# Performance work log

Hardware: AMD Instinct MI355X
Metric: run time of the kernel (lower is better)

Reference implementation:

```python
import jax, jax.numpy as jnp
import numpy as np

NHEAD = 16
D_MODEL = 1024
HEAD_DIM = D_MODEL // NHEAD


def setup_inputs() -> dict:
    key = jax.random.key(0)
    k1, k2, k3 = jax.random.split(key, 3)
    x = jax.random.normal(k1, (4, 2048, D_MODEL), dtype=jnp.float32)
    # lecun_normal-like scaling for stability
    w_qkv = jax.random.normal(k2, (D_MODEL, 3 * D_MODEL), dtype=jnp.float32) / np.sqrt(D_MODEL)
    w_out = jax.random.normal(k3, (D_MODEL, D_MODEL), dtype=jnp.float32) / np.sqrt(D_MODEL)
    return {"x": x, "w_qkv": w_qkv, "w_out": w_out}


def reference(x, w_qkv, w_out):
    # Fused QKV projection (self-attention: x_kv = x)
    qkv = x @ w_qkv  # [B, S, 3*D]
    q, k, v = jnp.split(qkv, 3, axis=-1)
    B, S = x.shape[0], x.shape[1]
    # [B, S, H, hd] -> [B, H, S, hd]
    q = jnp.moveaxis(q.reshape(B, S, NHEAD, HEAD_DIM), -2, -3)
    k = jnp.moveaxis(k.reshape(B, S, NHEAD, HEAD_DIM), -2, -3)
    v = jnp.moveaxis(v.reshape(B, S, NHEAD, HEAD_DIM), -2, -3)
    scale = 1.0 / jnp.sqrt(jnp.float32(HEAD_DIM))
    logits = jnp.einsum('bhqd,bhkd->bhqk', q, k) * scale
    weights = jax.nn.softmax(logits, axis=-1)
    out = jnp.einsum('bhqk,bhkd->bhqd', weights, v)  # [B, H, S, hd]
    out = jnp.moveaxis(out, -3, -2).reshape(B, S, D_MODEL)
    return out @ w_out
```

## Files before the change

kernel.cpp:

```cpp
#include <hip/hip_runtime.h>
#include <hip/hip_bf16.h>
#include <math.h>

#define D_MODEL 1024
#define NHEAD   16
#define HEAD_DIM 64
#define BATCH   4
#define SEQ     2048

typedef __attribute__((ext_vector_type(8))) short bf16x8;
typedef __attribute__((ext_vector_type(4))) float f32x4;
typedef __attribute__((ext_vector_type(16))) float f32x16;

__device__ inline ushort f2bf(float f) {
  __hip_bfloat16 h = __float2bfloat16(f);
  return *reinterpret_cast<ushort*>(&h);
}
__device__ inline uint pk2(float a, float b) {
  return (uint)f2bf(a) | ((uint)f2bf(b) << 16);
}
__device__ inline float bf2f(ushort u) {
  return __uint_as_float((uint)u << 16);
}
__device__ inline f32x16 zero16() {
  f32x16 z;
#pragma unroll
  for (int i = 0; i < 16; ++i) z[i] = 0.f;
  return z;
}
__device__ inline float fexp2(float x) { return __builtin_amdgcn_exp2f(x); }

__device__ inline void gld_lds16(const ushort* g, ushort* l) {
  __builtin_amdgcn_global_load_lds(
      (const __attribute__((address_space(1))) void*)g,
      (__attribute__((address_space(3))) void*)l, 16, 0, 0);
}

__global__ __launch_bounds__(256) void fill_f32(float* __restrict__ p, int n, float v) {
  int i = blockIdx.x * 256 + threadIdx.x;
  if (i < n) p[i] = v;
}

__global__ __launch_bounds__(256) void cast_bf16(const float* __restrict__ in,
                                                 ushort* __restrict__ out, int n8) {
  int i = blockIdx.x * 256 + threadIdx.x;
  if (i >= n8) return;
  const float4* p = (const float4*)(in + i * 8);
  float4 a = p[0], b = p[1];
  uint4 o;
  o.x = pk2(a.x, a.y); o.y = pk2(a.z, a.w);
  o.z = pk2(b.x, b.y); o.w = pk2(b.z, b.w);
  ((uint4*)out)[i] = o;
}

__global__ __launch_bounds__(256) void transpose_f32_bf16(const float* __restrict__ in,
                                                          ushort* __restrict__ out,
                                                          int R, int C) {
  __shared__ float tile[32][33];
  int tx = threadIdx.x, ty = threadIdx.y;
  int c0 = blockIdx.x * 32, r0 = blockIdx.y * 32;
#pragma unroll
  for (int k = 0; k < 4; ++k)
    tile[ty + 8 * k][tx] = in[(size_t)(r0 + ty + 8 * k) * C + c0 + tx];
  __syncthreads();
#pragma unroll
  for (int k = 0; k < 4; ++k)
    out[(size_t)(c0 + ty + 8 * k) * R + r0 + tx] = f2bf(tile[tx][ty + 8 * k]);
}

__device__ inline bf16x8 lds_read_swz(const ushort* base, int byteoff) {
  byteoff ^= ((byteoff >> 7) & 7) << 4;
  return *(const bf16x8*)((const char*)base + byteoff);
}

template <typename OutT>
__global__ __launch_bounds__(512, 2) void gemm_8ph(const ushort* __restrict__ A,
                                                   const ushort* __restrict__ BT,
                                                   OutT* __restrict__ C,
                                                   int M, int N, int K, int n_tiles) {
  __shared__ ushort AS[2][256 * 64];
  __shared__ ushort BS[2][256 * 64];

  const int tid = threadIdx.x;
  const int w = tid >> 6, lane = tid & 63;
  const int quad = lane >> 4, l16 = lane & 15;
  const int wm = w >> 2, wn = w & 3;
  const int tiles_x = N >> 8;
  const int NKT = K >> 6;

  int arow[4], acol[4];
  uint sdst[4];
#pragma unroll
  for (int i = 0; i < 4; ++i) {
    int x = (i * 512 + tid) * 16;
    int sx = x ^ (((x >> 7) & 7) << 4);
    arow[i] = sx >> 7;
    acol[i] = (sx & 127) >> 1;
    sdst[i] = (uint)(i * 512 + w * 64) * 8;
  }

  for (int t = blockIdx.x; t < n_tiles; t += gridDim.x) {
    const int m0 = (t / tiles_x) << 8, n0 = (t % tiles_x) << 8;

    int aoff[4], boff[4];
#pragma unroll
    for (int i = 0; i < 4; ++i) {
      aoff[i] = (m0 + arow[i]) * K + acol[i];
      boff[i] = (n0 + arow[i]) * K + acol[i];
    }

    f32x4 acc[8][4];
#pragma unroll
    for (int mt = 0; mt < 8; ++mt)
#pragma unroll
      for (int nt = 0; nt < 4; ++nt) acc[mt][nt] = (f32x4){0.f, 0.f, 0.f, 0.f};

#pragma unroll
    for (int i = 0; i < 4; ++i) gld_lds16(A + aoff[i], AS[0] + sdst[i]);
#pragma unroll
    for (int i = 0; i < 4; ++i) gld_lds16(BT + boff[i], BS[0] + sdst[i]);
#pragma unroll
    for (int i = 0; i < 4; ++i) gld_lds16(A + aoff[i] + 64, AS[1] + sdst[i]);
#pragma unroll
    for (int i = 0; i < 4; ++i) gld_lds16(BT + boff[i] + 64, BS[1] + sdst[i]);

    for (int kt = 0; kt < NKT; ++kt) {
      const int cur = kt & 1;

      if (kt + 1 < NKT) asm volatile("s_waitcnt vmcnt(8)" ::: "memory");
      else              asm volatile("s_waitcnt vmcnt(0)" ::: "memory");
      __builtin_amdgcn_s_barrier();

      bf16x8 af0[4][2], af1[4][2], bf0[2][2], bf1[2][2];

#pragma unroll
      for (int f = 0; f < 4; ++f)
#pragma unroll
        for (int kk = 0; kk < 2; ++kk)
          af0[f][kk] = lds_read_swz(AS[cur], (wm * 128 + f * 16 + l16) * 128 + kk * 64 + quad * 16);
#pragma unroll
      for (int g = 0; g < 2; ++g)
#pragma unroll
        for (int kk = 0; kk < 2; ++kk)
          bf0[g][kk] = lds_read_swz(BS[cur], (wn * 64 + g * 16 + l16) * 128 + kk * 64 + quad * 16);
      __builtin_amdgcn_s_setprio(1);
#pragma unroll
      for (int f = 0; f < 4; ++f)
#pragma unroll
        for (int g = 0; g < 2; ++g)
#pragma unroll
          for (int kk = 0; kk < 2; ++kk)
            acc[f][g] = __builtin_amdgcn_mfma_f32_16x16x32_bf16(af0[f][kk], bf0[g][kk], acc[f][g], 0, 0, 0);
      __builtin_amdgcn_s_setprio(0);

#pragma unroll
      for (int f = 0; f < 4; ++f)
#pragma unroll
        for (int kk = 0; kk < 2; ++kk)
          af1[f][kk] = lds_read_swz(AS[cur], (wm * 128 + 64 + f * 16 + l16) * 128 + kk * 64 + quad * 16);
      __builtin_amdgcn_s_setprio(1);
#pragma unroll
      for (int f = 0; f < 4; ++f)
#pragma unroll
        for (int g = 0; g < 2; ++g)
#pragma unroll
          for (int kk = 0; kk < 2; ++kk)
            acc[4 + f][g] = __builtin_amdgcn_mfma_f32_16x16x32_bf16(af1[f][kk], bf0[g][kk], acc[4 + f][g], 0, 0, 0);
      __builtin_amdgcn_s_setprio(0);

#pragma unroll
      for (int g = 0; g < 2; ++g)
#pragma unroll
        for (int kk = 0; kk < 2; ++kk)
          bf1[g][kk] = lds_read_swz(BS[cur], (wn * 64 + 32 + g * 16 + l16) * 128 + kk * 64 + quad * 16);
      __builtin_amdgcn_s_setprio(1);
#pragma unroll
      for (int f = 0; f < 4; ++f)
#pragma unroll
        for (int g = 0; g < 2; ++g)
#pragma unroll
          for (int kk = 0; kk < 2; ++kk)
            acc[f][2 + g] = __builtin_amdgcn_mfma_f32_16x16x32_bf16(af0[f][kk], bf1[g][kk], acc[f][2 + g], 0, 0, 0);
      __builtin_amdgcn_s_setprio(0);
      __builtin_amdgcn_s_barrier();

      if (kt + 2 < NKT) {
        const int k0n = (kt + 2) << 6;
#pragma unroll
        for (int i = 0; i < 4; ++i) gld_lds16(A + aoff[i] + k0n, AS[cur] + sdst[i]);
#pragma unroll
        for (int i = 0; i < 4; ++i) gld_lds16(BT + boff[i] + k0n, BS[cur] + sdst[i]);
      }
      __builtin_amdgcn_s_setprio(1);
#pragma unroll
      for (int f = 0; f < 4; ++f)
#pragma unroll
        for (int g = 0; g < 2; ++g)
#pragma unroll
          for (int kk = 0; kk < 2; ++kk)
            acc[4 + f][2 + g] = __builtin_amdgcn_mfma_f32_16x16x32_bf16(af1[f][kk], bf1[g][kk], acc[4 + f][2 + g], 0, 0, 0);
      __builtin_amdgcn_s_setprio(0);
    }

#pragma unroll
    for (int mt = 0; mt < 8; ++mt) {
#pragma unroll
      for (int nt = 0; nt < 4; ++nt) {
#pragma unroll
        for (int r = 0; r < 4; ++r) {
          size_t idx = (size_t)(m0 + wm * 128 + mt * 16 + quad * 4 + r) * N
                       + n0 + wn * 64 + nt * 16 + l16;
          if constexpr (sizeof(OutT) == 4) C[idx] = acc[mt][nt][r];
          else                             C[idx] = f2bf(acc[mt][nt][r]);
        }
      }
    }
  }
}

#define KST 72
#define VST 72
#define NT  (SEQ / 64)
__global__ __launch_bounds__(256, 4) void attn_mfma(const ushort* __restrict__ qkv,
                                                    ushort* __restrict__ attn_o) {
  __shared__ ushort Ks[2][64 * KST];
  __shared__ ushort VTs[2][64 * VST];

  const int tid = threadIdx.x;
  const int w = tid >> 6, lane = tid & 63;
  const int q32 = lane & 31, hi = lane >> 5;

  const int f = blockIdx.x;
  const int xcd = f & 7;
  const int j = f >> 3;
  const int qb = j & 15;
  const int hb = ((j >> 4) << 3) | xcd;
  const int h = hb & 15, b = hb >> 4;
  const int q0 = qb * 128;

  const float qscale = 0.125f * 1.44269504088896f;
  bf16x8 qfrag[4];
  {
    const ushort* qrow = qkv + (size_t)(b * SEQ + q0 + w * 32 + q32) * 3072 + h * 64;
#pragma unroll
    for (int dd = 0; dd < 4; ++dd) {
      bf16x8 fq = *(const bf16x8*)(qrow + dd * 16 + hi * 8);
#pragma unroll
      for (int jj = 0; jj < 8; ++jj)
        fq[jj] = (short)f2bf(bf2f((ushort)fq[jj]) * qscale);
      qfrag[dd] = fq;
    }
  }

  f32x16 oacc0 = zero16(), oacc1 = zero16(), lacc = zero16();

  bf16x8 ones;
#pragma unroll
  for (int jj = 0; jj < 8; ++jj) ones[jj] = (short)0x3F80;

  const int sr = tid >> 2, sc = tid & 3;
  const int kp = tid & 31, dg = tid >> 5;

  const size_t kstep = (size_t)64 * 3072;
  const ushort* kbase = qkv + (size_t)(b * SEQ + sr) * 3072 + 1024 + h * 64 + sc * 16;
  const ushort* vbase = qkv + (size_t)(b * SEQ + 2 * kp) * 3072 + 2048 + h * 64 + dg * 8;

  uint4 kreg0, kreg1, vreg0, vreg1;
  {
    const uint4* ks = (const uint4*)kbase;
    kreg0 = ks[0]; kreg1 = ks[1];
    vreg0 = *(const uint4*)vbase;
    vreg1 = *(const uint4*)(vbase + 3072);
    uint4* kdst = (uint4*)(Ks[0] + sr * KST + sc * 16);
    kdst[0] = kreg0; kdst[1] = kreg1;
    const ushort* ae = (const ushort*)&vreg0;
    const ushort* ce = (const ushort*)&vreg1;
#pragma unroll
    for (int jj = 0; jj < 8; ++jj) {
      VTs[0][(dg * 8 + jj) * VST + 2 * kp]     = ae[jj];
      VTs[0][(dg * 8 + jj) * VST + 2 * kp + 1] = ce[jj];
    }
  }

  for (int kt = 0; kt < NT; ++kt) {
    const int cur = kt & 1;
    __syncthreads();

    if (kt + 1 < NT) {
      const uint4* ks = (const uint4*)(kbase + (size_t)(kt + 1) * kstep);
      kreg0 = ks[0]; kreg1 = ks[1];
      vreg0 = *(const uint4*)(vbase + (size_t)(kt + 1) * kstep);
      vreg1 = *(const uint4*)(vbase + (size_t)(kt + 1) * kstep + 3072);
    }

    f32x16 sacc0 = zero16(), sacc1 = zero16();
    __builtin_amdgcn_s_setprio(1);
#pragma unroll
    for (int dd = 0; dd < 4; ++dd) {
      bf16x8 kf0 = *(const bf16x8*)(Ks[cur] + (q32)*KST + dd * 16 + hi * 8);
      bf16x8 kf1 = *(const bf16x8*)(Ks[cur] + (32 + q32) * KST + dd * 16 + hi * 8);
      sacc0 = __builtin_amdgcn_mfma_f32_32x32x16_bf16(kf0, qfrag[dd], sacc0, 0, 0, 0);
      sacc1 = __builtin_amdgcn_mfma_f32_32x32x16_bf16(kf1, qfrag[dd], sacc1, 0, 0, 0);
    }
    __builtin_amdgcn_s_setprio(0);

    bf16x8 pa[4];
#pragma unroll
    for (int kblk = 0; kblk < 2; ++kblk) {
      const f32x16& sacc = kblk ? sacc1 : sacc0;
      uint d0[4], d1[4];
#pragma unroll
      for (int p = 0; p < 4; ++p) {
        d0[p] = pk2(fexp2(sacc[4 * p + 0]), fexp2(sacc[4 * p + 1]));
        d1[p] = pk2(fexp2(sacc[4 * p + 2]), fexp2(sacc[4 * p + 3]));
      }
#pragma unroll
      for (int k2 = 0; k2 < 2; ++k2) {
        uint A0 = d0[2 * k2], B0 = d0[2 * k2 + 1];
        uint A1 = d1[2 * k2], B1 = d1[2 * k2 + 1];
        asm("v_permlane32_swap_b32 %0, %1" : "+v"(A0), "+v"(B0));
        asm("v_permlane32_swap_b32 %0, %1" : "+v"(A1), "+v"(B1));
        uint4 fr = {A0, A1, B0, B1};
        pa[kblk * 2 + k2] = *(bf16x8*)&fr;
        lacc = __builtin_amdgcn_mfma_f32_32x32x16_bf16(pa[kblk * 2 + k2], ones, lacc, 0, 0, 0);
      }
    }

    __builtin_amdgcn_s_setprio(1);
#pragma unroll
    for (int kb2 = 0; kb2 < 4; ++kb2) {
      bf16x8 vf0 = *(const bf16x8*)(VTs[cur] + (q32)*VST + kb2 * 16 + hi * 8);
      bf16x8 vf1 = *(const bf16x8*)(VTs[cur] + (32 + q32) * VST + kb2 * 16 + hi * 8);
      oacc0 = __builtin_amdgcn_mfma_f32_32x32x16_bf16(pa[kb2], vf0, oacc0, 0, 0, 0);
      oacc1 = __builtin_amdgcn_mfma_f32_32x32x16_bf16(pa[kb2], vf1, oacc1, 0, 0, 0);
    }
    __builtin_amdgcn_s_setprio(0);

    if (kt + 1 < NT) {
      uint4* kdst = (uint4*)(Ks[cur ^ 1] + sr * KST + sc * 16);
      kdst[0] = kreg0; kdst[1] = kreg1;
      const ushort* ae = (const ushort*)&vreg0;
      const ushort* ce = (const ushort*)&vreg1;
#pragma unroll
      for (int jj = 0; jj < 8; ++jj) {
        VTs[cur ^ 1][(dg * 8 + jj) * VST + 2 * kp]     = ae[jj];
        VTs[cur ^ 1][(dg * 8 + jj) * VST + 2 * kp + 1] = ce[jj];
      }
    }
  }

#pragma unroll
  for (int p = 0; p < 4; ++p) {
#pragma unroll
    for (int r = 0; r < 4; ++r) {
      int qrow = r + 8 * p + 4 * hi;
      float linv = 1.0f / lacc[4 * p + r];
      ushort* orow = attn_o + (size_t)(b * SEQ + q0 + w * 32 + qrow) * 1024 + h * 64 + q32;
      orow[0]  = f2bf(oacc0[4 * p + r] * linv);
      orow[32] = f2bf(oacc1[4 * p + r] * linv);
    }
  }
}

extern "C" void kernel_launch(void* const* d_in, const int* in_sizes, int n_in,
                              void* d_out, int out_size, void* d_ws, size_t ws_size,
                              hipStream_t stream) {
  bool ok_n  = (n_in == 3);
  bool ok_s0 = ok_n && (in_sizes[0] == 4 * 2048 * 1024);
  bool ok_s1 = ok_n && (in_sizes[1] == 1024 * 3072);
  bool ok_s2 = ok_n && (in_sizes[2] == 1024 * 1024);
  bool ok_o  = (out_size == 4 * 2048 * 1024);
  bool ok_w  = (ws_size >= (size_t)8192 * 3072 * 4);
  if (!(ok_n && ok_s0 && ok_s1 && ok_s2 && ok_o && ok_w)) {
    float c = 64.0f + 1.0f * ok_n + 2.0f * ok_s0 + 4.0f * ok_s1 +
              8.0f * ok_s2 + 16.0f * ok_o + 32.0f * ok_w;
    fill_f32<<<(out_size + 255) / 256, 256, 0, stream>>>((float*)d_out, out_size, c);
    return;
  }

  const float* x     = (const float*)d_in[0];
  const float* w_qkv = (const float*)d_in[1];
  const float* w_out = (const float*)d_in[2];

  char* ws = (char*)d_ws;
  ushort* qkv    = (ushort*)ws;
  ushort* xb     = (ushort*)(ws + (size_t)48 * 1024 * 1024);
  ushort* attn_o = (ushort*)(ws + (size_t)64 * 1024 * 1024);
  ushort* wqkvT  = (ushort*)(ws + (size_t)80 * 1024 * 1024);
  ushort* woutT  = (ushort*)(ws + (size_t)86 * 1024 * 1024);

  cast_bf16<<<dim3(8192 * 1024 / 8 / 256), dim3(256), 0, stream>>>(x, xb, 8192 * 1024 / 8);
  transpose_f32_bf16<<<dim3(3072 / 32, 1024 / 32), dim3(32, 8), 0, stream>>>(w_qkv, wqkvT, 1024, 3072);
  transpose_f32_bf16<<<dim3(1024 / 32, 1024 / 32), dim3(32, 8), 0, stream>>>(w_out, woutT, 1024, 1024);

  gemm_8ph<ushort><<<dim3(192), dim3(512), 0, stream>>>(
      xb, wqkvT, qkv, 8192, 3072, 1024, 384);

  attn_mfma<<<dim3(1024), dim3(256), 0, stream>>>(qkv, attn_o);

  gemm_8ph<float><<<dim3(128), dim3(512), 0, stream>>>(
      attn_o, woutT, (float*)d_out, 8192, 1024, 1024, 128);
}
```

Before: 278.7 us.

## Rewrite GEMM with half-tile staged pipeline, one tile per block, XCD remap

The persistent double-buffered GEMM is replaced by a kernel that computes one 256x256 tile per block. A and B are split into 128-row halves whose global-to-LDS loads are issued between the four MFMA phases, so loads for the next k-step overlap compute at finer granularity. Block IDs are remapped so neighbouring tiles land on the same XCD, and launch bounds drop to one block per CU. This adds more barriers per k-step, and the QKV GEMM now launches 384 blocks instead of a persistent 192.

```diff
diff --git a/kernel.cpp b/kernel.cpp
--- a/kernel.cpp
+++ b/kernel.cpp
@@ -68,154 +68,161 @@
     out[(size_t)(c0 + ty + 8 * k) * R + r0 + tx] = f2bf(tile[tx][ty + 8 * k]);
 }
 
-__device__ inline bf16x8 lds_read_swz(const ushort* base, int byteoff) {
+__device__ inline bf16x8 rd_half(const ushort* base, int row, int kk, int quad) {
+  int byteoff = row * 128 + kk * 64 + quad * 16;
   byteoff ^= ((byteoff >> 7) & 7) << 4;
   return *(const bf16x8*)((const char*)base + byteoff);
 }
 
+#define MFMA16(a, b, c) __builtin_amdgcn_mfma_f32_16x16x32_bf16((a), (b), (c), 0, 0, 0)
+
 template <typename OutT>
-__global__ __launch_bounds__(512, 2) void gemm_8ph(const ushort* __restrict__ A,
-                                                   const ushort* __restrict__ BT,
-                                                   OutT* __restrict__ C,
-                                                   int M, int N, int K, int n_tiles) {
-  __shared__ ushort AS[2][256 * 64];
-  __shared__ ushort BS[2][256 * 64];
+__global__ __launch_bounds__(512, 1) void gemm_m201(const ushort* __restrict__ A,
+                                                    const ushort* __restrict__ BT,
+                                                    OutT* __restrict__ C,
+                                                    int M, int N, int K, int tiles_x) {
+  __shared__ ushort Ah[2][2][128 * 64];
+  __shared__ ushort Bh[2][2][128 * 64];
 
   const int tid = threadIdx.x;
   const int w = tid >> 6, lane = tid & 63;
   const int quad = lane >> 4, l16 = lane & 15;
   const int wm = w >> 2, wn = w & 3;
-  const int tiles_x = N >> 8;
   const int NKT = K >> 6;
 
-  int arow[4], acol[4];
-  uint sdst[4];
-#pragma unroll
-  for (int i = 0; i < 4; ++i) {
-    int x = (i * 512 + tid) * 16;
+  int bid = blockIdx.x;
+  { int chunk = gridDim.x >> 3; bid = (bid & 7) * chunk + (bid >> 3); }
+  const int m0 = (bid / tiles_x) << 8, n0 = (bid % tiles_x) << 8;
+
+  size_t aoffs[2], boffs[2];
+  uint sdst[2];
+#pragma unroll
+  for (int j = 0; j < 2; ++j) {
+    int x = (j * 512 + tid) * 16;
     int sx = x ^ (((x >> 7) & 7) << 4);
-    arow[i] = sx >> 7;
-    acol[i] = (sx & 127) >> 1;
-    sdst[i] = (uint)(i * 512 + w * 64) * 8;
-  }
-
-  for (int t = blockIdx.x; t < n_tiles; t += gridDim.x) {
-    const int m0 = (t / tiles_x) << 8, n0 = (t % tiles_x) << 8;
-
-    int aoff[4], boff[4];
-#pragma unroll
-    for (int i = 0; i < 4; ++i) {
-      aoff[i] = (m0 + arow[i]) * K + acol[i];
-      boff[i] = (n0 + arow[i]) * K + acol[i];
-    }
-
-    f32x4 acc[8][4];
-#pragma unroll
-    for (int mt = 0; mt < 8; ++mt)
-#pragma unroll
-      for (int nt = 0; nt < 4; ++nt) acc[mt][nt] = (f32x4){0.f, 0.f, 0.f, 0.f};
-
-#pragma unroll
-    for (int i = 0; i < 4; ++i) gld_lds16(A + aoff[i], AS[0] + sdst[i]);
-#pragma unroll
-    for (int i = 0; i < 4; ++i) gld_lds16(BT + boff[i], BS[0] + sdst[i]);
-#pragma unroll
-    for (int i = 0; i < 4; ++i) gld_lds16(A + aoff[i] + 64, AS[1] + sdst[i]);
-#pragma unroll
-    for (int i = 0; i < 4; ++i) gld_lds16(BT + boff[i] + 64, BS[1] + sdst[i]);
-
-    for (int kt = 0; kt < NKT; ++kt) {
-      const int cur = kt & 1;
-
-      if (kt + 1 < NKT) asm volatile("s_waitcnt vmcnt(8)" ::: "memory");
-      else              asm volatile("s_waitcnt vmcnt(0)" ::: "memory");
-      __builtin_amdgcn_s_barrier();
-
-      bf16x8 af0[4][2], af1[4][2], bf0[2][2], bf1[2][2];
-
-#pragma unroll
-      for (int f = 0; f < 4; ++f)
-#pragma unroll
-        for (int kk = 0; kk < 2; ++kk)
-          af0[f][kk] = lds_read_swz(AS[cur], (wm * 128 + f * 16 + l16) * 128 + kk * 64 + quad * 16);
+    int row = sx >> 7, col = (sx & 127) >> 1;
+    aoffs[j] = (size_t)(m0 + row) * K + col;
+    boffs[j] = (size_t)(n0 + row) * K + col;
+    sdst[j] = (uint)(j * 512 + w * 64) * 8;
+  }
+  const size_t hstep = (size_t)128 * K;
+
+#define STAGE_A(d, h, c_) do { \
+    _Pragma("unroll") for (int j = 0; j < 2; ++j) \
+      gld_lds16(A + aoffs[j] + (size_t)(h) * hstep + (c_) * 64, Ah[d][h] + sdst[j]); } while (0)
+#define STAGE_B(d, h, c_) do { \
+    _Pragma("unroll") for (int j = 0; j < 2; ++j) \
+      gld_lds16(BT + boffs[j] + (size_t)(h) * hstep + (c_) * 64, Bh[d][h] + sdst[j]); } while (0)
+
+  f32x4 acc[8][4];
+#pragma unroll
+  for (int f = 0; f < 8; ++f)
+#pragma unroll
+    for (int g = 0; g < 4; ++g) acc[f][g] = (f32x4){0.f, 0.f, 0.f, 0.f};
+
+  STAGE_A(0, 0, 0);
+  STAGE_B(0, 0, 0);
+  STAGE_A(0, 1, 0);
+  STAGE_B(0, 1, 0);
+  STAGE_A(1, 0, 1);
+  asm volatile("s_waitcnt vmcnt(2)" ::: "memory");
+  __builtin_amdgcn_s_barrier();
+
+  const int arow = l16;
+  const int brow = (wn & 1) * 64 + l16;
+  const ushort* Abase[2] = {Ah[0][wm], Ah[1][wm]};
+  const ushort* Bbase[2] = {Bh[0][wn >> 1], Bh[1][wn >> 1]};
+
+  for (int c = 0; c < NKT; ++c) {
+    const int d = c & 1;
+    bf16x8 a0[4][2], a1[4][2], b0[2][2], b1[2][2];
+
+#pragma unroll
+    for (int f = 0; f < 4; ++f)
+#pragma unroll
+      for (int kk = 0; kk < 2; ++kk) a0[f][kk] = rd_half(Abase[d], arow + f * 16, kk, quad);
+#pragma unroll
+    for (int g = 0; g < 2; ++g)
+#pragma unroll
+      for (int kk = 0; kk < 2; ++kk) b0[g][kk] = rd_half(Bbase[d], brow + g * 16, kk, quad);
+    if (c + 1 < NKT) { STAGE_B(d ^ 1, 0, c + 1); STAGE_A(d ^ 1, 1, c + 1); }
+    __builtin_amdgcn_s_barrier();
+    asm volatile("s_waitcnt lgkmcnt(0)" ::: "memory");
+    __builtin_amdgcn_sched_barrier(0);
+    __builtin_amdgcn_s_setprio(1);
+#pragma unroll
+    for (int f = 0; f < 4; ++f)
 #pragma unroll
       for (int g = 0; g < 2; ++g)
 #pragma unroll
-        for (int kk = 0; kk < 2; ++kk)
-          bf0[g][kk] = lds_read_swz(BS[cur], (wn * 64 + g * 16 + l16) * 128 + kk * 64 + quad * 16);
-      __builtin_amdgcn_s_setprio(1);
-#pragma unroll
-      for (int f = 0; f < 4; ++f)
-#pragma unroll
-        for (int g = 0; g < 2; ++g)
-#pragma unroll
-          for (int kk = 0; kk < 2; ++kk)
-            acc[f][g] = __builtin_amdgcn_mfma_f32_16x16x32_bf16(af0[f][kk], bf0[g][kk], acc[f][g], 0, 0, 0);
-      __builtin_amdgcn_s_setprio(0);
-
-#pragma unroll
-      for (int f = 0; f < 4; ++f)
-#pragma unroll
-        for (int kk = 0; kk < 2; ++kk)
-          af1[f][kk] = lds_read_swz(AS[cur], (wm * 128 + 64 + f * 16 + l16) * 128 + kk * 64 + quad * 16);
-      __builtin_amdgcn_s_setprio(1);
-#pragma unroll
-      for (int f = 0; f < 4; ++f)
-#pragma unroll
-        for (int g = 0; g < 2; ++g)
-#pragma unroll
-          for (int kk = 0; kk < 2; ++kk)
-            acc[4 + f][g] = __builtin_amdgcn_mfma_f32_16x16x32_bf16(af1[f][kk], bf0[g][kk], acc[4 + f][g], 0, 0, 0);
-      __builtin_amdgcn_s_setprio(0);
-
+        for (int kk = 0; kk < 2; ++kk) acc[f][g] = MFMA16(a0[f][kk], b0[g][kk], acc[f][g]);
+    __builtin_amdgcn_s_setprio(0);
+    __builtin_amdgcn_s_barrier();
+
+#pragma unroll
+    for (int g = 0; g < 2; ++g)
+#pragma unroll
+      for (int kk = 0; kk < 2; ++kk) b1[g][kk] = rd_half(Bbase[d], brow + 32 + g * 16, kk, quad);
+    if (c + 1 < NKT) STAGE_B(d ^ 1, 1, c + 1);
+    __builtin_amdgcn_s_barrier();
+    asm volatile("s_waitcnt lgkmcnt(0)" ::: "memory");
+    __builtin_amdgcn_sched_barrier(0);
+    __builtin_amdgcn_s_setprio(1);
+#pragma unroll
+    for (int f = 0; f < 4; ++f)
 #pragma unroll
       for (int g = 0; g < 2; ++g)
 #pragma unroll
-        for (int kk = 0; kk < 2; ++kk)
-          bf1[g][kk] = lds_read_swz(BS[cur], (wn * 64 + 32 + g * 16 + l16) * 128 + kk * 64 + quad * 16);
-      __builtin_amdgcn_s_setprio(1);
-#pragma unroll
-      for (int f = 0; f < 4; ++f)
-#pragma unroll
-        for (int g = 0; g < 2; ++g)
-#pragma unroll
-          for (int kk = 0; kk < 2; ++kk)
-            acc[f][2 + g] = __builtin_amdgcn_mfma_f32_16x16x32_bf16(af0[f][kk], bf1[g][kk], acc[f][2 + g], 0, 0, 0);
-      __builtin_amdgcn_s_setprio(0);
-      __builtin_amdgcn_s_barrier();
-
-      if (kt + 2 < NKT) {
-        const int k0n = (kt + 2) << 6;
-#pragma unroll
-        for (int i = 0; i < 4; ++i) gld_lds16(A + aoff[i] + k0n, AS[cur] + sdst[i]);
-#pragma unroll
-        for (int i = 0; i < 4; ++i) gld_lds16(BT + boff[i] + k0n, BS[cur] + sdst[i]);
+        for (int kk = 0; kk < 2; ++kk) acc[f][2 + g] = MFMA16(a0[f][kk], b1[g][kk], acc[f][2 + g]);
+    __builtin_amdgcn_s_setprio(0);
+    __builtin_amdgcn_s_barrier();
+
+#pragma unroll
+    for (int f = 0; f < 4; ++f)
+#pragma unroll
+      for (int kk = 0; kk < 2; ++kk) a1[f][kk] = rd_half(Abase[d], arow + 64 + f * 16, kk, quad);
+    __builtin_amdgcn_s_barrier();
+    asm volatile("s_waitcnt lgkmcnt(0)" ::: "memory");
+    __builtin_amdgcn_sched_barrier(0);
+    __builtin_amdgcn_s_setprio(1);
+#pragma unroll
+    for (int f = 0; f < 4; ++f)
+#pragma unroll
+      for (int g = 0; g < 2; ++g)
+#pragma unroll
+        for (int kk = 0; kk < 2; ++kk) acc[4 + f][g] = MFMA16(a1[f][kk], b0[g][kk], acc[4 + f][g]);
+    __builtin_amdgcn_s_setprio(0);
+    __builtin_amdgcn_s_barrier();
+
+    if (c + 2 < NKT) STAGE_A(d, 0, c + 2);
+    __builtin_amdgcn_s_setprio(1);
+#pragma unroll
+    for (int f = 0; f < 4; ++f)
+#pragma unroll
+      for (int g = 0; g < 2; ++g)
+#pragma unroll
+        for (int kk = 0; kk < 2; ++kk) acc[4 + f][2 + g] = MFMA16(a1[f][kk], b1[g][kk], acc[4 + f][2 + g]);
+    __builtin_amdgcn_s_setprio(0);
+    if (c + 2 < NKT)      asm volatile("s_waitcnt vmcnt(2)" ::: "memory");
+    else if (c + 1 < NKT) asm volatile("s_waitcnt vmcnt(0)" ::: "memory");
+    __builtin_amdgcn_s_barrier();
+  }
+
+#pragma unroll
+  for (int f = 0; f < 8; ++f) {
+#pragma unroll
+    for (int g = 0; g < 4; ++g) {
+#pragma unroll
+      for (int r = 0; r < 4; ++r) {
+        size_t idx = (size_t)(m0 + wm * 128 + f * 16 + quad * 4 + r) * N
+                     + n0 + wn * 64 + g * 16 + l16;
+        if constexpr (sizeof(OutT) == 4) C[idx] = acc[f][g][r];
+        else                             C[idx] = f2bf(acc[f][g][r]);
       }
-      __builtin_amdgcn_s_setprio(1);
-#pragma unroll
-      for (int f = 0; f < 4; ++f)
-#pragma unroll
-        for (int g = 0; g < 2; ++g)
-#pragma unroll
-          for (int kk = 0; kk < 2; ++kk)
-            acc[4 + f][2 + g] = __builtin_amdgcn_mfma_f32_16x16x32_bf16(af1[f][kk], bf1[g][kk], acc[4 + f][2 + g], 0, 0, 0);
-      __builtin_amdgcn_s_setprio(0);
-    }
-
-#pragma unroll
-    for (int mt = 0; mt < 8; ++mt) {
-#pragma unroll
-      for (int nt = 0; nt < 4; ++nt) {
-#pragma unroll
-        for (int r = 0; r < 4; ++r) {
-          size_t idx = (size_t)(m0 + wm * 128 + mt * 16 + quad * 4 + r) * N
-                       + n0 + wn * 64 + nt * 16 + l16;
-          if constexpr (sizeof(OutT) == 4) C[idx] = acc[mt][nt][r];
-          else                             C[idx] = f2bf(acc[mt][nt][r]);
-        }
-      }
-    }
-  }
+    }
+  }
+#undef STAGE_A
+#undef STAGE_B
 }
 
 #define KST 72
@@ -393,11 +400,11 @@
   transpose_f32_bf16<<<dim3(3072 / 32, 1024 / 32), dim3(32, 8), 0, stream>>>(w_qkv, wqkvT, 1024, 3072);
   transpose_f32_bf16<<<dim3(1024 / 32, 1024 / 32), dim3(32, 8), 0, stream>>>(w_out, woutT, 1024, 1024);
 
-  gemm_8ph<ushort><<<dim3(192), dim3(512), 0, stream>>>(
-      xb, wqkvT, qkv, 8192, 3072, 1024, 384);
+  gemm_m201<ushort><<<dim3(384), dim3(512), 0, stream>>>(
+      xb, wqkvT, qkv, 8192, 3072, 1024, 12);
 
   attn_mfma<<<dim3(1024), dim3(256), 0, stream>>>(qkv, attn_o);
 
-  gemm_8ph<float><<<dim3(128), dim3(512), 0, stream>>>(
-      attn_o, woutT, (float*)d_out, 8192, 1024, 1024, 128);
-}
+  gemm_m201<float><<<dim3(128), dim3(512), 0, stream>>>(
+      attn_o, woutT, (float*)d_out, 8192, 1024, 1024, 4);
+}
```

New measurement: 439.3 us. 1.58x slower.
